# Kernel tuning notes

Hardware: AMD Instinct MI355X
Metric: run time of the kernel (lower is better)

Reference implementation:

```python
import jax, jax.numpy as jnp
import numpy as np

N = 50000
E = 800000
EPS = 1e-5


def gcn_conv(x, W, b, src, dst, n):
    # PyG GCNConv: h = xW; add self-loops; symmetric norm D^-1/2 A_hat D^-1/2; out = agg + bias
    h = x @ W                                            # [N, out]
    deg = jax.ops.segment_sum(jnp.ones_like(src, dtype=h.dtype), dst, num_segments=n) + 1.0
    inv_sqrt = jax.lax.rsqrt(deg)                        # [N]
    coef = inv_sqrt[src] * inv_sqrt[dst]                 # [E]
    agg = jax.ops.segment_sum(h[src] * coef[:, None], dst, num_segments=n)
    agg = agg + h * (inv_sqrt * inv_sqrt)[:, None]       # self-loop term
    return agg + b


def batchnorm(h, gamma, beta):
    mean = jnp.mean(h, axis=0)
    var = jnp.var(h, axis=0)
    return gamma * (h - mean) * jax.lax.rsqrt(var + EPS) + beta


def setup_inputs() -> dict:
    key = jax.random.key(0)
    ks = jax.random.split(key, 8)
    x = jax.random.normal(ks[0], (N, 128), dtype=jnp.float32)
    edge_index = jax.random.randint(ks[1], (2, E), 0, N, dtype=jnp.int64)
    s = 1.0 / np.sqrt(128)
    W1 = jax.random.uniform(ks[2], (128, 128), jnp.float32, -s, s)
    W2 = jax.random.uniform(ks[3], (128, 128), jnp.float32, -s, s)
    W3 = jax.random.uniform(ks[4], (128, 64), jnp.float32, -s, s)
    b1 = jnp.zeros((128,), jnp.float32)
    b2 = jnp.zeros((128,), jnp.float32)
    b3 = jnp.zeros((64,), jnp.float32)
    g1 = jnp.ones((128,), jnp.float32)
    bt1 = jnp.zeros((128,), jnp.float32)
    g2 = jnp.ones((128,), jnp.float32)
    bt2 = jnp.zeros((128,), jnp.float32)
    return {"x": x, "edge_index": edge_index, "W1": W1, "b1": b1, "g1": g1, "bt1": bt1,
            "W2": W2, "b2": b2, "g2": g2, "bt2": bt2, "W3": W3, "b3": b3}


def reference(x, edge_index, W1, b1, g1, bt1, W2, b2, g2, bt2, W3, b3):
    src, dst = edge_index[0], edge_index[1]
    h = gcn_conv(x, W1, b1, src, dst, N)
    h = jax.nn.relu(batchnorm(h, g1, bt1))
    h = gcn_conv(h, W2, b2, src, dst, N)
    h = jax.nn.relu(batchnorm(h, g2, bt2))
    out = gcn_conv(h, W3, b3, src, dst, N)
    return out
```

## Files before the change

kernel.cpp:

```cpp
#include <hip/hip_runtime.h>

#define N_NODES 50000
#define N_EDGES 800000
static constexpr float EPS = 1e-5f;
static constexpr int NCH   = 16;
static constexpr int EPC   = N_EDGES / NCH;
static constexpr int NW    = (N_NODES + 3) / 4;
static constexpr int SCAN_NB = (N_NODES + 1023) / 1024;
static constexpr int GEMM_NB = (N_NODES + 127) / 128;
static constexpr int FILL_NB = (N_EDGES + 1023) / 1024;
static constexpr int WCONV_NB = 160;

using bf16x8 = __attribute__((ext_vector_type(8))) short;
using f32x4  = __attribute__((ext_vector_type(4))) float;

static __device__ __forceinline__ unsigned short f2bf(float f) {
    unsigned int u = __float_as_uint(f);
    return (unsigned short)((u + 0x7FFFu + ((u >> 16) & 1u)) >> 16);
}
static __device__ __forceinline__ float blo(unsigned int w) { return __uint_as_float(w << 16); }
static __device__ __forceinline__ float bhi(unsigned int w) { return __uint_as_float(w & 0xffff0000u); }

__global__ __launch_bounds__(256) void k_hist_wconv(
    const int* __restrict__ ei, unsigned char* __restrict__ rank8,
    unsigned int* __restrict__ basesU,
    const float* __restrict__ W1, const float* __restrict__ W2,
    const float* __restrict__ W3,
    unsigned short* __restrict__ Wf1, unsigned short* __restrict__ Wf2,
    unsigned short* __restrict__ Wf3, int4* __restrict__ statz) {
    __shared__ unsigned int h[NW];
    const int t = threadIdx.x;
    if (blockIdx.x < NCH) {
        for (int i = t; i < NW; i += 256) h[i] = 0;
        __syncthreads();
        const int cbeg = blockIdx.x * EPC;
        for (int e0 = cbeg + t * 4; e0 < cbeg + EPC; e0 += 1024) {
            int4 d4 = *(const int4*)&ei[N_EDGES + e0];
            int sh0 = (d4.x & 3) * 8, sh1 = (d4.y & 3) * 8;
            int sh2 = (d4.z & 3) * 8, sh3 = (d4.w & 3) * 8;
            unsigned int o0 = atomicAdd(&h[d4.x >> 2], 1u << sh0);
            unsigned int o1 = atomicAdd(&h[d4.y >> 2], 1u << sh1);
            unsigned int o2 = atomicAdd(&h[d4.z >> 2], 1u << sh2);
            unsigned int o3 = atomicAdd(&h[d4.w >> 2], 1u << sh3);
            unsigned int pk = ((o0 >> sh0) & 0xffu) | (((o1 >> sh1) & 0xffu) << 8)
                            | (((o2 >> sh2) & 0xffu) << 16) | (((o3 >> sh3) & 0xffu) << 24);
            *(unsigned int*)&rank8[e0] = pk;
        }
        __syncthreads();
        for (int i = t; i < NW; i += 256)
            basesU[blockIdx.x * NW + i] = h[i];
    } else {
        int gid = (blockIdx.x - NCH) * 256 + t;
        if (gid < 128) statz[gid] = make_int4(0, 0, 0, 0);
        const float* W; unsigned short* Wf; int NCOL, idx;
        if (gid < 16384)      { W = W1; Wf = Wf1; NCOL = 128; idx = gid; }
        else if (gid < 32768) { W = W2; Wf = Wf2; NCOL = 128; idx = gid - 16384; }
        else                  { W = W3; Wf = Wf3; NCOL = 64;  idx = gid - 32768; }
        int j  = idx & 7;
        int l  = (idx >> 3) & 63;
        int s  = (idx >> 9) & 3;
        int tn = idx >> 11;
        int n = tn * 16 + (l & 15);
        int k = s * 32 + (l >> 4) * 8 + j;
        Wf[idx] = f2bf(W[k * NCOL + n]);
    }
}

template <int NCOL, bool BN, bool ABF16>
static __device__ __forceinline__ void gemm_body(
    int row0, int t,
    const void* __restrict__ Ap, const unsigned short* __restrict__ Wf,
    const float* __restrict__ stats,
    const float* __restrict__ gamma, const float* __restrict__ beta,
    unsigned short* __restrict__ H,
    unsigned short* As, float* sc_s, float* sh_s) {
    if (BN) {
        if (t < 128) {
            float s  = stats[t];
            float sq = stats[128 + t];
            float mean = s * (1.0f / N_NODES);
            float var  = sq * (1.0f / N_NODES) - mean * mean;
            float sc = gamma[t] * rsqrtf(var + EPS);
            sc_s[t] = sc;
            sh_s[t] = beta[t] - mean * sc;
        }
        __syncthreads();
    }

#pragma unroll
    for (int i = 0; i < 8; i++) {
        int q = i * 256 + t;
        int row = q >> 4;
        int c8  = (q & 15) * 8;
        int grow = row0 + row;
        float v[8];
        if (grow < N_NODES) {
            if (ABF16) {
                uint4 p = *(const uint4*)((const unsigned short*)Ap + (size_t)grow * 128 + c8);
                v[0] = blo(p.x); v[1] = bhi(p.x); v[2] = blo(p.y); v[3] = bhi(p.y);
                v[4] = blo(p.z); v[5] = bhi(p.z); v[6] = blo(p.w); v[7] = bhi(p.w);
            } else {
                const float* Af = (const float*)Ap + (size_t)grow * 128 + c8;
                float4 f0 = *(const float4*)Af;
                float4 f1 = *(const float4*)(Af + 4);
                v[0] = f0.x; v[1] = f0.y; v[2] = f0.z; v[3] = f0.w;
                v[4] = f1.x; v[5] = f1.y; v[6] = f1.z; v[7] = f1.w;
            }
        } else {
#pragma unroll
            for (int j = 0; j < 8; j++) v[j] = 0.f;
        }
        if (BN) {
#pragma unroll
            for (int j = 0; j < 8; j++)
                v[j] = fmaxf(fmaf(v[j], sc_s[c8 + j], sh_s[c8 + j]), 0.f);
        }
        uint4 pk;
        pk.x = (unsigned)f2bf(v[0]) | ((unsigned)f2bf(v[1]) << 16);
        pk.y = (unsigned)f2bf(v[2]) | ((unsigned)f2bf(v[3]) << 16);
        pk.z = (unsigned)f2bf(v[4]) | ((unsigned)f2bf(v[5]) << 16);
        pk.w = (unsigned)f2bf(v[6]) | ((unsigned)f2bf(v[7]) << 16);
        *(uint4*)&As[row * 136 + c8] = pk;
    }
    __syncthreads();

    const int wv = t >> 6;
    const int l  = t & 63;
    const int m  = l & 15;
    const int kq = l >> 4;

    bf16x8 a0[4], a1[4];
    const unsigned short* ar0 = &As[(wv * 32 + m) * 136 + kq * 8];
    const unsigned short* ar1 = &As[(wv * 32 + 16 + m) * 136 + kq * 8];
#pragma unroll
    for (int s = 0; s < 4; s++) {
        a0[s] = *(const bf16x8*)(ar0 + s * 32);
        a1[s] = *(const bf16x8*)(ar1 + s * 32);
    }
    __syncthreads();

    constexpr int NT = NCOL / 16;
#pragma unroll
    for (int tn = 0; tn < NT; tn++) {
        f32x4 c0 = {0.f, 0.f, 0.f, 0.f};
        f32x4 c1 = {0.f, 0.f, 0.f, 0.f};
#pragma unroll
        for (int s = 0; s < 4; s++) {
            bf16x8 b = *(const bf16x8*)&Wf[(size_t)((tn * 4 + s) * 64 + l) * 8];
            c0 = __builtin_amdgcn_mfma_f32_16x16x32_bf16(a0[s], b, c0, 0, 0, 0);
            c1 = __builtin_amdgcn_mfma_f32_16x16x32_bf16(a1[s], b, c1, 0, 0, 0);
        }
        int col = tn * 16 + m;
#pragma unroll
        for (int r = 0; r < 4; r++) {
            As[(wv * 32 + kq * 4 + r) * 136 + col]      = f2bf(c0[r]);
            As[(wv * 32 + 16 + kq * 4 + r) * 136 + col] = f2bf(c1[r]);
        }
    }
    __syncthreads();

    constexpr int GPR  = NCOL / 8;
    constexpr int ITER = 128 * GPR / 256;
#pragma unroll
    for (int i = 0; i < ITER; i++) {
        int q = i * 256 + t;
        int row = q / GPR;
        int c8  = (q % GPR) * 8;
        int grow = row0 + row;
        if (grow < N_NODES) {
            uint4 pk = *(const uint4*)&As[row * 136 + c8];
            *(uint4*)&H[(size_t)grow * NCOL + c8] = pk;
        }
    }
    __syncthreads();
}

template <int NCOL>
__global__ __launch_bounds__(256) void k_gemm_bn(
    const unsigned short* __restrict__ A, const unsigned short* __restrict__ Wf,
    const float* __restrict__ stats,
    const float* __restrict__ gamma, const float* __restrict__ beta,
    unsigned short* __restrict__ H) {
    __shared__ unsigned short As[128 * 136];
    __shared__ float sc_s[128], sh_s[128];
    gemm_body<NCOL, true, true>(blockIdx.x * 128, threadIdx.x, A, Wf, stats,
                                gamma, beta, H, As, sc_s, sh_s);
}

__global__ __launch_bounds__(256) void k_gemm1_scan1(
    const float* __restrict__ x, const unsigned short* __restrict__ Wf1,
    unsigned short* __restrict__ h1,
    unsigned int* __restrict__ basesU, float* __restrict__ inv_sqrt,
    int* __restrict__ excl, int* __restrict__ partials) {
    __shared__ unsigned short As[128 * 136];
    __shared__ float sc_s[128], sh_s[128];
    const int t = threadIdx.x;
    if (blockIdx.x < GEMM_NB) {
        gemm_body<128, false, false>(blockIdx.x * 128, t, x, Wf1,
                                     nullptr, nullptr, nullptr, h1, As, sc_s, sh_s);
    } else {
        int* shi = (int*)As;
        const int g = (blockIdx.x - GEMM_NB) * 256 + t;
        int r0 = 0, r1 = 0, r2 = 0, r3 = 0;
        if (g < NW) {
#pragma unroll
            for (int c = 0; c < NCH; c++) {
                unsigned int w = basesU[c * NW + g];
                unsigned int pb = (unsigned)r0 | ((unsigned)r1 << 8)
                                | ((unsigned)r2 << 16) | ((unsigned)r3 << 24);
                basesU[c * NW + g] = pb;
                r0 += w & 0xff; r1 += (w >> 8) & 0xff;
                r2 += (w >> 16) & 0xff; r3 += (w >> 24) & 0xff;
            }
        }
        int S = r0 + r1 + r2 + r3;
        shi[t] = S;
        __syncthreads();
        for (int off = 1; off < 256; off <<= 1) {
            int u = (t >= off) ? shi[t - off] : 0;
            __syncthreads();
            shi[t] += u;
            __syncthreads();
        }
        int base = shi[t] - S;
        if (g < NW) {
            int i0 = g * 4;
            *(int4*)&excl[i0] = make_int4(base, base + r0, base + r0 + r1,
                                          base + r0 + r1 + r2);
            *(float4*)&inv_sqrt[i0] = make_float4(
                rsqrtf((float)r0 + 1.0f), rsqrtf((float)r1 + 1.0f),
                rsqrtf((float)r2 + 1.0f), rsqrtf((float)r3 + 1.0f));
        }
        if (t == 255) partials[blockIdx.x - GEMM_NB] = shi[t];
    }
}

__global__ __launch_bounds__(256) void k_scan2_fill(
    const int* __restrict__ excl, const int* __restrict__ partials,
    int* __restrict__ rowptr,
    const int* __restrict__ ei, const unsigned char* __restrict__ rank8,
    const unsigned char* __restrict__ cb8,
    int* __restrict__ esrc) {
    const int t = threadIdx.x;
    __shared__ int sh[256];
    __shared__ int ps[256];
    int v = (t < SCAN_NB) ? partials[t] : 0;
    sh[t] = v;
    __syncthreads();
    for (int off = 1; off < 256; off <<= 1) {
        int u = (t >= off) ? sh[t - off] : 0;
        __syncthreads();
        sh[t] += u;
        __syncthreads();
    }
    ps[t] = sh[t] - v;
    __syncthreads();

    if (blockIdx.x < SCAN_NB) {
        int i0 = (blockIdx.x * 256 + t) * 4;
        if (i0 < N_NODES) {
            int4 e4 = *(const int4*)&excl[i0];
            int b = ps[blockIdx.x];
            *(int4*)&rowptr[i0] = make_int4(e4.x + b, e4.y + b, e4.z + b, e4.w + b);
        }
        if (blockIdx.x == 0 && t == 0) rowptr[N_NODES] = N_EDGES;
    } else {
        int e0 = ((blockIdx.x - SCAN_NB) * 256 + t) * 4;
        if (e0 < N_EDGES) {
            const int c = e0 / EPC;
            const unsigned char* cb = cb8 + (size_t)c * N_NODES;
            int4 s4 = *(const int4*)&ei[e0];
            int4 d4 = *(const int4*)&ei[N_EDGES + e0];
            unsigned int r4 = *(const unsigned int*)&rank8[e0];
            int p0 = excl[d4.x] + ps[d4.x >> 10] + cb[d4.x] + (r4 & 0xff);
            int p1 = excl[d4.y] + ps[d4.y >> 10] + cb[d4.y] + ((r4 >> 8) & 0xff);
            int p2 = excl[d4.z] + ps[d4.z >> 10] + cb[d4.z] + ((r4 >> 16) & 0xff);
            int p3 = excl[d4.w] + ps[d4.w >> 10] + cb[d4.w] + ((r4 >> 24) & 0xff);
            esrc[p0] = s4.x;
            esrc[p1] = s4.y;
            esrc[p2] = s4.z;
            esrc[p3] = s4.w;
        }
    }
}

template <int F, bool OUTBF>
__global__ __launch_bounds__(256) void k_agg(const int* __restrict__ rowptr,
                                             const int* __restrict__ esrc,
                                             const float* __restrict__ inv_sqrt,
                                             const unsigned short* __restrict__ H,
                                             const float* __restrict__ bias,
                                             void* __restrict__ OUT) {
    constexpr int LPN = F / 8;
    constexpr int NPB = 256 / LPN;
    const int t = threadIdx.x;
    const int node = blockIdx.x * NPB + t / LPN;
    const int lane = t % LPN;
    if (node >= N_NODES) return;

    const uint4* __restrict__ Hv = (const uint4*)H;
    const int beg = rowptr[node];
    const int end = rowptr[node + 1];
    const float rsn = inv_sqrt[node];

    float acc[8];
#pragma unroll
    for (int i = 0; i < 8; i++) acc[i] = 0.f;

#define ACC8(P, C)                                                     \
    acc[0] = fmaf(blo((P).x), (C), acc[0]);                            \
    acc[1] = fmaf(bhi((P).x), (C), acc[1]);                            \
    acc[2] = fmaf(blo((P).y), (C), acc[2]);                            \
    acc[3] = fmaf(bhi((P).y), (C), acc[3]);                            \
    acc[4] = fmaf(blo((P).z), (C), acc[4]);                            \
    acc[5] = fmaf(bhi((P).z), (C), acc[5]);                            \
    acc[6] = fmaf(blo((P).w), (C), acc[6]);                            \
    acc[7] = fmaf(bhi((P).w), (C), acc[7]);

    int j = beg;
    for (; j + 7 < end; j += 8) {
        int4 sa = *(const int4*)&esrc[j];
        int4 sb = *(const int4*)&esrc[j + 4];
        uint4 p0 = Hv[(size_t)sa.x * LPN + lane];
        uint4 p1 = Hv[(size_t)sa.y * LPN + lane];
        uint4 p2 = Hv[(size_t)sa.z * LPN + lane];
        uint4 p3 = Hv[(size_t)sa.w * LPN + lane];
        uint4 p4 = Hv[(size_t)sb.x * LPN + lane];
        uint4 p5 = Hv[(size_t)sb.y * LPN + lane];
        uint4 p6 = Hv[(size_t)sb.z * LPN + lane];
        uint4 p7 = Hv[(size_t)sb.w * LPN + lane];
        float c0 = inv_sqrt[sa.x] * rsn, c1 = inv_sqrt[sa.y] * rsn;
        float c2 = inv_sqrt[sa.z] * rsn, c3 = inv_sqrt[sa.w] * rsn;
        float c4 = inv_sqrt[sb.x] * rsn, c5 = inv_sqrt[sb.y] * rsn;
        float c6 = inv_sqrt[sb.z] * rsn, c7 = inv_sqrt[sb.w] * rsn;
        ACC8(p0, c0) ACC8(p1, c1) ACC8(p2, c2) ACC8(p3, c3)
        ACC8(p4, c4) ACC8(p5, c5) ACC8(p6, c6) ACC8(p7, c7)
    }
    if (j + 3 < end) {
        int4 sa = *(const int4*)&esrc[j];
        uint4 p0 = Hv[(size_t)sa.x * LPN + lane];
        uint4 p1 = Hv[(size_t)sa.y * LPN + lane];
        uint4 p2 = Hv[(size_t)sa.z * LPN + lane];
        uint4 p3 = Hv[(size_t)sa.w * LPN + lane];
        float c0 = inv_sqrt[sa.x] * rsn, c1 = inv_sqrt[sa.y] * rsn;
        float c2 = inv_sqrt[sa.z] * rsn, c3 = inv_sqrt[sa.w] * rsn;
        ACC8(p0, c0) ACC8(p1, c1) ACC8(p2, c2) ACC8(p3, c3)
        j += 4;
    }
    for (; j < end; j++) {
        int s0 = esrc[j];
        float c0 = inv_sqrt[s0] * rsn;
        uint4 p0 = Hv[(size_t)s0 * LPN + lane];
        ACC8(p0, c0)
    }
#undef ACC8

    uint4 ps = Hv[(size_t)node * LPN + lane];
    float idv = rsn * rsn;
    float4 b0 = ((const float4*)bias)[lane * 2];
    float4 b1 = ((const float4*)bias)[lane * 2 + 1];
    acc[0] = fmaf(blo(ps.x), idv, acc[0]) + b0.x;
    acc[1] = fmaf(bhi(ps.x), idv, acc[1]) + b0.y;
    acc[2] = fmaf(blo(ps.y), idv, acc[2]) + b0.z;
    acc[3] = fmaf(bhi(ps.y), idv, acc[3]) + b0.w;
    acc[4] = fmaf(blo(ps.z), idv, acc[4]) + b1.x;
    acc[5] = fmaf(bhi(ps.z), idv, acc[5]) + b1.y;
    acc[6] = fmaf(blo(ps.w), idv, acc[6]) + b1.z;
    acc[7] = fmaf(bhi(ps.w), idv, acc[7]) + b1.w;

    if (OUTBF) {
        uint4 pk;
        pk.x = (unsigned)f2bf(acc[0]) | ((unsigned)f2bf(acc[1]) << 16);
        pk.y = (unsigned)f2bf(acc[2]) | ((unsigned)f2bf(acc[3]) << 16);
        pk.z = (unsigned)f2bf(acc[4]) | ((unsigned)f2bf(acc[5]) << 16);
        pk.w = (unsigned)f2bf(acc[6]) | ((unsigned)f2bf(acc[7]) << 16);
        ((uint4*)OUT)[(size_t)node * LPN + lane] = pk;
    } else {
        float4* o = (float4*)OUT + ((size_t)node * LPN + lane) * 2;
        o[0] = make_float4(acc[0], acc[1], acc[2], acc[3]);
        o[1] = make_float4(acc[4], acc[5], acc[6], acc[7]);
    }
}

__global__ __launch_bounds__(256) void k_stats(const unsigned short* __restrict__ A,
                                               float* __restrict__ stats) {
    const int t  = threadIdx.x;
    const int c4 = t & 31;
    const int rr = t >> 5;
    float4 sum = make_float4(0.f, 0.f, 0.f, 0.f);
    float4 sq  = make_float4(0.f, 0.f, 0.f, 0.f);
    for (int row = blockIdx.x * 8 + rr; row < N_NODES; row += gridDim.x * 8) {
        uint2 p = *(const uint2*)&A[(size_t)row * 128 + c4 * 4];
        float vx = blo(p.x), vy = bhi(p.x), vz = blo(p.y), vw = bhi(p.y);
        sum.x += vx; sum.y += vy; sum.z += vz; sum.w += vw;
        sq.x += vx * vx; sq.y += vy * vy; sq.z += vz * vz; sq.w += vw * vw;
    }
    __shared__ float4 red[2][8][32];
    red[0][rr][c4] = sum;
    red[1][rr][c4] = sq;
    __syncthreads();
    if (t < 32) {
        float4 s = make_float4(0.f, 0.f, 0.f, 0.f);
        float4 q = make_float4(0.f, 0.f, 0.f, 0.f);
#pragma unroll
        for (int i = 0; i < 8; i++) {
            float4 a = red[0][i][t];
            float4 b = red[1][i][t];
            s.x += a.x; s.y += a.y; s.z += a.z; s.w += a.w;
            q.x += b.x; q.y += b.y; q.z += b.z; q.w += b.w;
        }
        int c = t * 4;
        atomicAdd(&stats[c + 0], s.x); atomicAdd(&stats[c + 1], s.y);
        atomicAdd(&stats[c + 2], s.z); atomicAdd(&stats[c + 3], s.w);
        atomicAdd(&stats[128 + c + 0], q.x); atomicAdd(&stats[128 + c + 1], q.y);
        atomicAdd(&stats[128 + c + 2], q.z); atomicAdd(&stats[128 + c + 3], q.w);
    }
}

extern "C" void kernel_launch(void* const* d_in, const int* in_sizes, int n_in,
                              void* d_out, int out_size, void* d_ws, size_t ws_size,
                              hipStream_t stream) {
    const float* x   = (const float*)d_in[0];
    const int*   ei  = (const int*)d_in[1];
    const float* W1  = (const float*)d_in[2];
    const float* b1  = (const float*)d_in[3];
    const float* g1  = (const float*)d_in[4];
    const float* bt1 = (const float*)d_in[5];
    const float* W2  = (const float*)d_in[6];
    const float* b2  = (const float*)d_in[7];
    const float* g2  = (const float*)d_in[8];
    const float* bt2 = (const float*)d_in[9];
    const float* W3  = (const float*)d_in[10];
    const float* b3  = (const float*)d_in[11];
    float* out = (float*)d_out;

    char* ws = (char*)d_ws;
    size_t off = 0;
    auto alloc = [&](size_t bytes) { char* p = ws + off; off += (bytes + 255) & ~(size_t)255; return p; };
    float* stats1   = (float*)alloc(256 * 4);
    float* stats2   = (float*)alloc(256 * 4);
    unsigned int*  basesU = (unsigned int*)alloc((size_t)NCH * NW * 4);
    unsigned char* rank8  = (unsigned char*)alloc((size_t)N_EDGES);
    float* inv_sqrt = (float*)alloc((size_t)N_NODES * 4);
    int*   excl     = (int*)  alloc((size_t)N_NODES * 4);
    int*   partials = (int*)  alloc(256 * 4);
    int*   rowptr   = (int*)  alloc((size_t)(N_NODES + 1) * 4);
    int*   esrc     = (int*)  alloc((size_t)N_EDGES * 4);
    unsigned short* Wf1 = (unsigned short*)alloc((size_t)128 * 128 * 2);
    unsigned short* Wf2 = (unsigned short*)alloc((size_t)128 * 128 * 2);
    unsigned short* Wf3 = (unsigned short*)alloc((size_t)64 * 128 * 2);
    unsigned short* h1  = (unsigned short*)alloc((size_t)N_NODES * 128 * 2);
    unsigned short* h2  = (unsigned short*)alloc((size_t)N_NODES * 128 * 2);
    unsigned short* h3  = (unsigned short*)alloc((size_t)N_NODES * 64 * 2);
    unsigned short* agg1 = (unsigned short*)alloc((size_t)N_NODES * 128 * 2);
    unsigned short* agg2 = (unsigned short*)alloc((size_t)N_NODES * 128 * 2);

    k_hist_wconv<<<NCH + WCONV_NB, 256, 0, stream>>>(ei, rank8, basesU,
                                                     W1, W2, W3, Wf1, Wf2, Wf3,
                                                     (int4*)stats1);
    k_gemm1_scan1<<<GEMM_NB + SCAN_NB, 256, 0, stream>>>(x, Wf1, h1, basesU,
                                                         inv_sqrt, excl, partials);
    k_scan2_fill<<<SCAN_NB + FILL_NB, 256, 0, stream>>>(excl, partials, rowptr,
                                                        ei, rank8,
                                                        (const unsigned char*)basesU,
                                                        esrc);
    k_agg<128, true><<<N_NODES / 16, 256, 0, stream>>>(rowptr, esrc, inv_sqrt, h1, b1, agg1);
    k_stats<<<256, 256, 0, stream>>>(agg1, stats1);
    k_gemm_bn<128><<<GEMM_NB, 256, 0, stream>>>(agg1, Wf2, stats1, g1, bt1, h2);
    k_agg<128, true><<<N_NODES / 16, 256, 0, stream>>>(rowptr, esrc, inv_sqrt, h2, b2, agg2);
    k_stats<<<256, 256, 0, stream>>>(agg2, stats2);
    k_gemm_bn<64><<<GEMM_NB, 256, 0, stream>>>(agg2, Wf3, stats2, g2, bt2, h3);
    k_agg<64, false><<<(N_NODES + 31) / 32, 256, 0, stream>>>(rowptr, esrc, inv_sqrt, h3, b3, out);
}
```

Before: 302.3 us.

## Double histogram chunks, precompute per-chunk int bases, widen stats loads

After: 258.0 us. 14.7% less time.

```diff
diff --git a/kernel.cpp b/kernel.cpp
--- a/kernel.cpp
+++ b/kernel.cpp
@@ -3,7 +3,7 @@
 #define N_NODES 50000
 #define N_EDGES 800000
 static constexpr float EPS = 1e-5f;
-static constexpr int NCH   = 16;
+static constexpr int NCH   = 32;
 static constexpr int EPC   = N_EDGES / NCH;
 static constexpr int NW    = (N_NODES + 3) / 4;
 static constexpr int SCAN_NB = (N_NODES + 1023) / 1024;
@@ -23,7 +23,7 @@
 
 __global__ __launch_bounds__(256) void k_hist_wconv(
     const int* __restrict__ ei, unsigned char* __restrict__ rank8,
-    unsigned int* __restrict__ basesU,
+    unsigned int* __restrict__ hcnt,
     const float* __restrict__ W1, const float* __restrict__ W2,
     const float* __restrict__ W3,
     unsigned short* __restrict__ Wf1, unsigned short* __restrict__ Wf2,
@@ -48,7 +48,7 @@
         }
         __syncthreads();
         for (int i = t; i < NW; i += 256)
-            basesU[blockIdx.x * NW + i] = h[i];
+            hcnt[blockIdx.x * NW + i] = h[i];
     } else {
         int gid = (blockIdx.x - NCH) * 256 + t;
         if (gid < 128) statz[gid] = make_int4(0, 0, 0, 0);
@@ -190,7 +190,8 @@
 __global__ __launch_bounds__(256) void k_gemm1_scan1(
     const float* __restrict__ x, const unsigned short* __restrict__ Wf1,
     unsigned short* __restrict__ h1,
-    unsigned int* __restrict__ basesU, float* __restrict__ inv_sqrt,
+    const unsigned int* __restrict__ hcnt, int* __restrict__ cbase32,
+    float* __restrict__ inv_sqrt,
     int* __restrict__ excl, int* __restrict__ partials) {
     __shared__ unsigned short As[128 * 136];
     __shared__ float sc_s[128], sh_s[128];
@@ -202,13 +203,15 @@
         int* shi = (int*)As;
         const int g = (blockIdx.x - GEMM_NB) * 256 + t;
         int r0 = 0, r1 = 0, r2 = 0, r3 = 0;
+        unsigned int cnt[NCH];
         if (g < NW) {
 #pragma unroll
+            for (int c = 0; c < NCH; c++) cnt[c] = hcnt[c * NW + g];
+#pragma unroll
             for (int c = 0; c < NCH; c++) {
-                unsigned int w = basesU[c * NW + g];
-                unsigned int pb = (unsigned)r0 | ((unsigned)r1 << 8)
-                                | ((unsigned)r2 << 16) | ((unsigned)r3 << 24);
-                basesU[c * NW + g] = pb;
+                unsigned int w = cnt[c];
+                cnt[c] = (unsigned)r0 | ((unsigned)r1 << 8)
+                       | ((unsigned)r2 << 16) | ((unsigned)r3 << 24);
                 r0 += w & 0xff; r1 += (w >> 8) & 0xff;
                 r2 += (w >> 16) & 0xff; r3 += (w >> 24) & 0xff;
             }
@@ -225,11 +228,18 @@
         int base = shi[t] - S;
         if (g < NW) {
             int i0 = g * 4;
-            *(int4*)&excl[i0] = make_int4(base, base + r0, base + r0 + r1,
-                                          base + r0 + r1 + r2);
+            int e0 = base, e1 = base + r0, e2 = base + r0 + r1, e3 = base + r0 + r1 + r2;
+            *(int4*)&excl[i0] = make_int4(e0, e1, e2, e3);
             *(float4*)&inv_sqrt[i0] = make_float4(
                 rsqrtf((float)r0 + 1.0f), rsqrtf((float)r1 + 1.0f),
                 rsqrtf((float)r2 + 1.0f), rsqrtf((float)r3 + 1.0f));
+#pragma unroll
+            for (int c = 0; c < NCH; c++) {
+                unsigned int pb = cnt[c];
+                *(int4*)&cbase32[c * N_NODES + i0] = make_int4(
+                    e0 + (int)(pb & 0xff), e1 + (int)((pb >> 8) & 0xff),
+                    e2 + (int)((pb >> 16) & 0xff), e3 + (int)((pb >> 24) & 0xff));
+            }
         }
         if (t == 255) partials[blockIdx.x - GEMM_NB] = shi[t];
     }
@@ -239,7 +249,7 @@
     const int* __restrict__ excl, const int* __restrict__ partials,
     int* __restrict__ rowptr,
     const int* __restrict__ ei, const unsigned char* __restrict__ rank8,
-    const unsigned char* __restrict__ cb8,
+    const int* __restrict__ cbase32,
     int* __restrict__ esrc) {
     const int t = threadIdx.x;
     __shared__ int sh[256];
@@ -267,15 +277,14 @@
     } else {
         int e0 = ((blockIdx.x - SCAN_NB) * 256 + t) * 4;
         if (e0 < N_EDGES) {
-            const int c = e0 / EPC;
-            const unsigned char* cb = cb8 + (size_t)c * N_NODES;
+            const int* cb = cbase32 + (e0 / EPC) * N_NODES;
             int4 s4 = *(const int4*)&ei[e0];
             int4 d4 = *(const int4*)&ei[N_EDGES + e0];
             unsigned int r4 = *(const unsigned int*)&rank8[e0];
-            int p0 = excl[d4.x] + ps[d4.x >> 10] + cb[d4.x] + (r4 & 0xff);
-            int p1 = excl[d4.y] + ps[d4.y >> 10] + cb[d4.y] + ((r4 >> 8) & 0xff);
-            int p2 = excl[d4.z] + ps[d4.z >> 10] + cb[d4.z] + ((r4 >> 16) & 0xff);
-            int p3 = excl[d4.w] + ps[d4.w >> 10] + cb[d4.w] + ((r4 >> 24) & 0xff);
+            int p0 = cb[d4.x] + ps[d4.x >> 10] + (r4 & 0xff);
+            int p1 = cb[d4.y] + ps[d4.y >> 10] + ((r4 >> 8) & 0xff);
+            int p2 = cb[d4.z] + ps[d4.z >> 10] + ((r4 >> 16) & 0xff);
+            int p3 = cb[d4.w] + ps[d4.w >> 10] + ((r4 >> 24) & 0xff);
             esrc[p0] = s4.x;
             esrc[p1] = s4.y;
             esrc[p2] = s4.z;
@@ -385,35 +394,38 @@
 __global__ __launch_bounds__(256) void k_stats(const unsigned short* __restrict__ A,
                                                float* __restrict__ stats) {
     const int t  = threadIdx.x;
-    const int c4 = t & 31;
-    const int rr = t >> 5;
-    float4 sum = make_float4(0.f, 0.f, 0.f, 0.f);
-    float4 sq  = make_float4(0.f, 0.f, 0.f, 0.f);
-    for (int row = blockIdx.x * 8 + rr; row < N_NODES; row += gridDim.x * 8) {
-        uint2 p = *(const uint2*)&A[(size_t)row * 128 + c4 * 4];
-        float vx = blo(p.x), vy = bhi(p.x), vz = blo(p.y), vw = bhi(p.y);
-        sum.x += vx; sum.y += vy; sum.z += vz; sum.w += vw;
-        sq.x += vx * vx; sq.y += vy * vy; sq.z += vz * vz; sq.w += vw * vw;
-    }
-    __shared__ float4 red[2][8][32];
-    red[0][rr][c4] = sum;
-    red[1][rr][c4] = sq;
-    __syncthreads();
-    if (t < 32) {
-        float4 s = make_float4(0.f, 0.f, 0.f, 0.f);
-        float4 q = make_float4(0.f, 0.f, 0.f, 0.f);
-#pragma unroll
-        for (int i = 0; i < 8; i++) {
-            float4 a = red[0][i][t];
-            float4 b = red[1][i][t];
-            s.x += a.x; s.y += a.y; s.z += a.z; s.w += a.w;
-            q.x += b.x; q.y += b.y; q.z += b.z; q.w += b.w;
-        }
-        int c = t * 4;
-        atomicAdd(&stats[c + 0], s.x); atomicAdd(&stats[c + 1], s.y);
-        atomicAdd(&stats[c + 2], s.z); atomicAdd(&stats[c + 3], s.w);
-        atomicAdd(&stats[128 + c + 0], q.x); atomicAdd(&stats[128 + c + 1], q.y);
-        atomicAdd(&stats[128 + c + 2], q.z); atomicAdd(&stats[128 + c + 3], q.w);
+    const int c8 = t & 15;
+    const int rr = t >> 4;
+    float sum[8] = {0,0,0,0,0,0,0,0};
+    float sq[8]  = {0,0,0,0,0,0,0,0};
+    for (int row = blockIdx.x * 16 + rr; row < N_NODES; row += gridDim.x * 16) {
+        uint4 p = *(const uint4*)&A[(size_t)row * 128 + c8 * 8];
+        float v[8] = {blo(p.x), bhi(p.x), blo(p.y), bhi(p.y),
+                      blo(p.z), bhi(p.z), blo(p.w), bhi(p.w)};
+#pragma unroll
+        for (int i = 0; i < 8; i++) { sum[i] += v[i]; sq[i] += v[i] * v[i]; }
+    }
+    __shared__ float red[16][16][8];
+#pragma unroll
+    for (int i = 0; i < 8; i++) red[rr][c8][i] = sum[i];
+    __syncthreads();
+    if (t < 128) {
+        int g = t >> 3, i = t & 7;
+        float s = 0.f;
+#pragma unroll
+        for (int r = 0; r < 16; r++) s += red[r][g][i];
+        atomicAdd(&stats[g * 8 + i], s);
+    }
+    __syncthreads();
+#pragma unroll
+    for (int i = 0; i < 8; i++) red[rr][c8][i] = sq[i];
+    __syncthreads();
+    if (t < 128) {
+        int g = t >> 3, i = t & 7;
+        float s = 0.f;
+#pragma unroll
+        for (int r = 0; r < 16; r++) s += red[r][g][i];
+        atomicAdd(&stats[128 + g * 8 + i], s);
     }
 }
 
@@ -439,7 +451,8 @@
     auto alloc = [&](size_t bytes) { char* p = ws + off; off += (bytes + 255) & ~(size_t)255; return p; };
     float* stats1   = (float*)alloc(256 * 4);
     float* stats2   = (float*)alloc(256 * 4);
-    unsigned int*  basesU = (unsigned int*)alloc((size_t)NCH * NW * 4);
+    unsigned int* hcnt   = (unsigned int*)alloc((size_t)NCH * NW * 4);
+    int*          cbase32 = (int*)alloc((size_t)NCH * N_NODES * 4);
     unsigned char* rank8  = (unsigned char*)alloc((size_t)N_EDGES);
     float* inv_sqrt = (float*)alloc((size_t)N_NODES * 4);
     int*   excl     = (int*)  alloc((size_t)N_NODES * 4);
@@ -455,15 +468,14 @@
     unsigned short* agg1 = (unsigned short*)alloc((size_t)N_NODES * 128 * 2);
     unsigned short* agg2 = (unsigned short*)alloc((size_t)N_NODES * 128 * 2);
 
-    k_hist_wconv<<<NCH + WCONV_NB, 256, 0, stream>>>(ei, rank8, basesU,
+    k_hist_wconv<<<NCH + WCONV_NB, 256, 0, stream>>>(ei, rank8, hcnt,
                                                      W1, W2, W3, Wf1, Wf2, Wf3,
                                                      (int4*)stats1);
-    k_gemm1_scan1<<<GEMM_NB + SCAN_NB, 256, 0, stream>>>(x, Wf1, h1, basesU,
-                                                         inv_sqrt, excl, partials);
+    k_gemm1_scan1<<<GEMM_NB + SCAN_NB, 256, 0, stream>>>(x, Wf1, h1, hcnt,
+                                                         cbase32, inv_sqrt,
+                                                         excl, partials);
     k_scan2_fill<<<SCAN_NB + FILL_NB, 256, 0, stream>>>(excl, partials, rowptr,
-                                                        ei, rank8,
-                                                        (const unsigned char*)basesU,
-                                                        esrc);
+                                                        ei, rank8, cbase32, esrc);
     k_agg<128, true><<<N_NODES / 16, 256, 0, stream>>>(rowptr, esrc, inv_sqrt, h1, b1, agg1);
     k_stats<<<256, 256, 0, stream>>>(agg1, stats1);
     k_gemm_bn<128><<<GEMM_NB, 256, 0, stream>>>(agg1, Wf2, stats1, g1, bt1, h2);
```
